# Performance work log

Hardware: AMD Instinct MI355X
Metric: run time of the kernel (lower is better)

The kernel has to match this reference:

```python
import jax, jax.numpy as jnp
import numpy as np

D_MODEL = 2048
N_HEADS = 16
D_HEAD = D_MODEL // N_HEADS
BATCH = 4
SEQ = 2048


def setup_inputs() -> dict:
    key = jax.random.key(0)
    ks = jax.random.split(key, 10)
    s = 1.0 / np.sqrt(D_MODEL)
    inp = {
        "x": jax.random.normal(ks[0], (BATCH, SEQ, D_MODEL), dtype=jnp.float32),
        "attn_mask": jnp.ones((1, 1, SEQ, SEQ), dtype=jnp.int32),
        "Wq": jax.random.uniform(ks[1], (D_MODEL, D_MODEL), jnp.float32, -s, s),
        "bq": jax.random.uniform(ks[2], (D_MODEL,), jnp.float32, -s, s),
        "Wk": jax.random.uniform(ks[3], (D_MODEL, D_MODEL), jnp.float32, -s, s),
        "bk": jax.random.uniform(ks[4], (D_MODEL,), jnp.float32, -s, s),
        "Wv": jax.random.uniform(ks[5], (D_MODEL, D_MODEL), jnp.float32, -s, s),
        "bv": jax.random.uniform(ks[6], (D_MODEL,), jnp.float32, -s, s),
        "Wo": jax.random.uniform(ks[7], (D_MODEL, D_MODEL), jnp.float32, -s, s),
        "bo": jax.random.uniform(ks[8], (D_MODEL,), jnp.float32, -s, s),
    }
    return inp


def reference(x, attn_mask, Wq, bq, Wk, bk, Wv, bv, Wo, bo):
    B, S, D = x.shape
    # projections (torch Linear: x @ W.T + b); split heads -> (B, H, S, Dh)
    def split(t):
        return t.reshape(B, S, N_HEADS, D_HEAD).transpose(0, 2, 1, 3)
    q = split(x @ Wq.T + bq)
    k = split(x @ Wk.T + bk)
    v = split(x @ Wv.T + bv)
    scale = 1.0 / np.sqrt(D_HEAD).astype(np.float32)
    scores = jnp.einsum('bhqd,bhkd->bhqk', q, k) * scale  # (B,H,S,S)
    scores = jnp.where(attn_mask == 0, jnp.float32(-jnp.inf), scores)
    attn = jax.nn.softmax(scores, axis=-1)
    out = jnp.einsum('bhqk,bhkd->bhqd', attn, v)  # (B,H,S,Dh)
    out = out.transpose(0, 2, 1, 3).reshape(B, S, D)
    return out @ Wo.T + bo
```

## Files before the change

### kernel.cpp

```cpp
#include <hip/hip_runtime.h>
#include <stdint.h>
#include <stddef.h>

typedef __attribute__((ext_vector_type(8))) short short8;
typedef __attribute__((ext_vector_type(4))) float f32x4;

#define SEQ    2048
#define DMODEL 2048
#define NHEAD  16
#define DHEAD  128
#define BATCH  4
#define KVT    32
#define NKVT   (SEQ / KVT)

__device__ __forceinline__ unsigned short f2b(float f) {
  unsigned int u;
  __builtin_memcpy(&u, &f, sizeof(u));
  u = u + 0x7FFFu + ((u >> 16) & 1u);
  return (unsigned short)(u >> 16);
}

__device__ __forceinline__ void gload16(const void* g, void* l) {
  __builtin_amdgcn_global_load_lds(
      (const __attribute__((address_space(1))) unsigned int*)g,
      (__attribute__((address_space(3))) unsigned int*)l, 16, 0, 0);
}

__global__ __launch_bounds__(256) void cvt_x_kernel(
    const float* __restrict__ src, unsigned short* __restrict__ dst, int n8)
{
  const int i = blockIdx.x * 256 + threadIdx.x;
  if (i >= n8) return;
  const f32x4 a = *(const f32x4*)(src + (size_t)i * 8);
  const f32x4 b = *(const f32x4*)(src + (size_t)i * 8 + 4);
  short8 o;
  o[0] = (short)f2b(a[0]); o[1] = (short)f2b(a[1]);
  o[2] = (short)f2b(a[2]); o[3] = (short)f2b(a[3]);
  o[4] = (short)f2b(b[0]); o[5] = (short)f2b(b[1]);
  o[6] = (short)f2b(b[2]); o[7] = (short)f2b(b[3]);
  *(short8*)(dst + (size_t)i * 8) = o;
}

__global__ __launch_bounds__(256) void cvt_w_kernel(
    const float* __restrict__ s0, const float* __restrict__ s1,
    const float* __restrict__ s2, const float* __restrict__ s3,
    unsigned short* __restrict__ dst, int n8)
{
  const int y = blockIdx.y;
  const float* src = (y == 0) ? s0 : (y == 1) ? s1 : (y == 2) ? s2 : s3;
  unsigned short* d = dst + (size_t)y * DMODEL * DMODEL;
  const int i = blockIdx.x * 256 + threadIdx.x;
  if (i >= n8) return;
  const f32x4 a = *(const f32x4*)(src + (size_t)i * 8);
  const f32x4 b = *(const f32x4*)(src + (size_t)i * 8 + 4);
  short8 o;
  o[0] = (short)f2b(a[0]); o[1] = (short)f2b(a[1]);
  o[2] = (short)f2b(a[2]); o[3] = (short)f2b(a[3]);
  o[4] = (short)f2b(b[0]); o[5] = (short)f2b(b[1]);
  o[6] = (short)f2b(b[2]); o[7] = (short)f2b(b[3]);
  *(short8*)(d + (size_t)i * 8) = o;
}

__global__ __launch_bounds__(256) void gemm_bt_kernel(
    const unsigned short* __restrict__ A,
    const unsigned short* __restrict__ W0, const unsigned short* __restrict__ W1,
    const unsigned short* __restrict__ W2,
    const float* __restrict__ b0, const float* __restrict__ b1,
    const float* __restrict__ b2,
    unsigned short* __restrict__ o0, unsigned short* __restrict__ o1,
    unsigned short* __restrict__ o2,
    float* __restrict__ of,
    int mode_base)
{
  const int z = blockIdx.z;
  const unsigned short* W    = (z == 0) ? W0 : (z == 1) ? W1 : W2;
  const float* bias          = (z == 0) ? b0 : (z == 1) ? b1 : b2;
  unsigned short* out        = (z == 0) ? o0 : (z == 1) ? o1 : o2;
  const int mode = mode_base + z;

  const int m0 = blockIdx.y * 128;
  const int n0 = blockIdx.x * 128;

  __shared__ __align__(16) unsigned short As[128 * 32];
  __shared__ __align__(16) unsigned short Bs[128 * 32];

  const int tid  = threadIdx.x;
  const int wave = tid >> 6;
  const int lane = tid & 63;
  const int l15  = lane & 15;
  const int lg   = lane >> 4;
  const int wr   = wave >> 1;
  const int wc   = wave & 1;

  f32x4 acc[4][4];
#pragma unroll
  for (int m = 0; m < 4; ++m)
#pragma unroll
    for (int n = 0; n < 4; ++n) acc[m][n] = (f32x4){0.f, 0.f, 0.f, 0.f};

  for (int kt = 0; kt < 64; ++kt) {
    const int k0 = kt * 32;
#pragma unroll
    for (int is = 0; is < 2; ++is) {
      const int f   = (is * 256 + tid) * 16;
      const int row = f >> 6;
      const int off = f & 63;
      gload16((const char*)(A + (size_t)(m0 + row) * DMODEL + k0) + off, (char*)As + f);
      gload16((const char*)(W + (size_t)(n0 + row) * DMODEL + k0) + off, (char*)Bs + f);
    }
    __syncthreads();

    short8 af[4], bfr[4];
#pragma unroll
    for (int m = 0; m < 4; ++m)
      af[m] = *(const short8*)(As + (wr * 64 + m * 16 + l15) * 32 + lg * 8);
#pragma unroll
    for (int n = 0; n < 4; ++n)
      bfr[n] = *(const short8*)(Bs + (wc * 64 + n * 16 + l15) * 32 + lg * 8);

#pragma unroll
    for (int m = 0; m < 4; ++m)
#pragma unroll
      for (int n = 0; n < 4; ++n)
        acc[m][n] = __builtin_amdgcn_mfma_f32_16x16x32_bf16(af[m], bfr[n], acc[m][n], 0, 0, 0);

    __syncthreads();
  }

#pragma unroll
  for (int n = 0; n < 4; ++n) {
    const int j = n0 + wc * 64 + n * 16 + l15;
    const float bb = bias[j];
#pragma unroll
    for (int m = 0; m < 4; ++m) {
#pragma unroll
      for (int r = 0; r < 4; ++r) {
        const int i = m0 + wr * 64 + m * 16 + lg * 4 + r;
        float v = acc[m][n][r] + bb;
        if (mode == 0) v *= 0.0883883476483184f;
        if (mode == 3) {
          of[(size_t)i * DMODEL + j] = v;
        } else {
          const int b = i >> 11, s = i & 2047, hh = j >> 7, dh = j & 127;
          const size_t bhOff = (size_t)(b * 16 + hh) * (SEQ * DHEAD);
          size_t addr;
          if (mode == 0)
            addr = bhOff + (size_t)s * DHEAD + dh;
          else if (mode == 1)
            addr = bhOff + (size_t)(s >> 4) * 2048 + (dh >> 5) * 512
                 + ((dh >> 3) & 3) * 128 + (s & 15) * 8 + (dh & 7);
          else
            addr = bhOff + (size_t)(s >> 5) * 4096 + (dh >> 4) * 512
                 + ((s >> 3) & 3) * 128 + (dh & 15) * 8 + (s & 7);
          out[addr] = f2b(v);
        }
      }
    }
  }
}

__global__ __launch_bounds__(256, 4) void attn_kernel(
    const unsigned short* __restrict__ Q,
    const unsigned short* __restrict__ Kf,
    const unsigned short* __restrict__ Vf,
    unsigned short* __restrict__ AO)
{
  const int idx = blockIdx.x;
  const int xcd = idx & 7;
  const int sq  = idx >> 3;
  const int bh  = xcd * 8 + (sq >> 5);
  const int qt  = sq & 31;

  const int wave = threadIdx.x >> 6;
  const int lane = threadIdx.x & 63;
  const int l15  = lane & 15;
  const int lg   = lane >> 4;
  const int q0   = qt * 64 + wave * 16;

  const unsigned short* Qb = Q  + (size_t)bh * SEQ * DHEAD;
  const unsigned short* Kb = Kf + (size_t)bh * SEQ * DHEAD;
  const unsigned short* Vb = Vf + (size_t)bh * SEQ * DHEAD;

  __shared__ __align__(16) unsigned short Ks[2][4096];
  __shared__ __align__(16) unsigned short Vs[2][4096];
  __shared__ __align__(16) unsigned short P[4][16][40];

  short8 qf[4];
#pragma unroll
  for (int k = 0; k < 4; ++k)
    qf[k] = *(const short8*)(Qb + (size_t)(q0 + l15) * DHEAD + k * 32 + lg * 8);

  short8 onesf;
#pragma unroll
  for (int e = 0; e < 8; ++e) onesf[e] = (short)0x3F80;

  f32x4 oacc[9];
#pragma unroll
  for (int n = 0; n < 9; ++n) oacc[n] = (f32x4){0.f, 0.f, 0.f, 0.f};
  float mrun[4];
#pragma unroll
  for (int r = 0; r < 4; ++r) mrun[r] = -1e30f;

  const int t = threadIdx.x;
  auto STAGE = [&](int buf, int kvt) {
    const unsigned short* ksrc = Kb + (size_t)kvt * 4096;
    const unsigned short* vsrc = Vb + (size_t)kvt * 4096;
    gload16(ksrc + t * 8,        &Ks[buf][t * 8]);
    gload16(ksrc + 2048 + t * 8, &Ks[buf][2048 + t * 8]);
    gload16(vsrc + t * 8,        &Vs[buf][t * 8]);
    gload16(vsrc + 2048 + t * 8, &Vs[buf][2048 + t * 8]);
  };

  STAGE(0, 0);

  for (int kvt = 0; kvt < NKVT; ++kvt) {
    const int cur = kvt & 1;
    if (kvt + 1 < NKVT) {
      STAGE(cur ^ 1, kvt + 1);
      asm volatile("s_waitcnt vmcnt(4)" ::: "memory");
    } else {
      asm volatile("s_waitcnt vmcnt(0)" ::: "memory");
    }
    __builtin_amdgcn_s_barrier();
    __builtin_amdgcn_sched_barrier(0);

    f32x4 sacc[2];
#pragma unroll
    for (int n = 0; n < 2; ++n) sacc[n] = (f32x4){0.f, 0.f, 0.f, 0.f};
    __builtin_amdgcn_s_setprio(1);
#pragma unroll
    for (int n = 0; n < 2; ++n) {
#pragma unroll
      for (int k = 0; k < 4; ++k) {
        short8 kfr = *(const short8*)(&Ks[cur][n * 2048 + k * 512 + lane * 8]);
        sacc[n] = __builtin_amdgcn_mfma_f32_16x16x32_bf16(qf[k], kfr, sacc[n], 0, 0, 0);
      }
    }
    __builtin_amdgcn_s_setprio(0);

    float d = -1e30f;
#pragma unroll
    for (int r = 0; r < 4; ++r)
      d = fmaxf(d, fmaxf(sacc[0][r], sacc[1][r]) - mrun[r]);
    if (__any(d > 8.f)) {
#pragma unroll
      for (int r = 0; r < 4; ++r) {
        float m = fmaxf(sacc[0][r], sacc[1][r]);
        m = fmaxf(m, __shfl_xor(m, 1));
        m = fmaxf(m, __shfl_xor(m, 2));
        m = fmaxf(m, __shfl_xor(m, 4));
        m = fmaxf(m, __shfl_xor(m, 8));
        if (m > mrun[r]) {
          const float alpha = __expf(mrun[r] - m);
#pragma unroll
          for (int n = 0; n < 9; ++n) oacc[n][r] *= alpha;
          mrun[r] = m;
        }
      }
    }

#pragma unroll
    for (int n = 0; n < 2; ++n)
#pragma unroll
      for (int r = 0; r < 4; ++r)
        P[wave][lg * 4 + r][n * 16 + l15] =
            (unsigned short)f2b(__expf(sacc[n][r] - mrun[r]));
    asm volatile("s_waitcnt lgkmcnt(0)" ::: "memory");
    __builtin_amdgcn_sched_barrier(0);

    short8 pf = *(const short8*)(&P[wave][l15][lg * 8]);
    __builtin_amdgcn_s_setprio(1);
#pragma unroll
    for (int n = 0; n < 8; ++n) {
      short8 vfr = *(const short8*)(&Vs[cur][n * 512 + lane * 8]);
      oacc[n] = __builtin_amdgcn_mfma_f32_16x16x32_bf16(pf, vfr, oacc[n], 0, 0, 0);
    }
    oacc[8] = __builtin_amdgcn_mfma_f32_16x16x32_bf16(pf, onesf, oacc[8], 0, 0, 0);
    __builtin_amdgcn_s_setprio(0);

    asm volatile("s_waitcnt lgkmcnt(0)" ::: "memory");
    __builtin_amdgcn_s_barrier();
    __builtin_amdgcn_sched_barrier(0);
  }

  const int b = bh >> 4, h = bh & 15;
  float inv[4];
#pragma unroll
  for (int r = 0; r < 4; ++r) inv[r] = 1.f / oacc[8][r];
#pragma unroll
  for (int n = 0; n < 8; ++n) {
#pragma unroll
    for (int r = 0; r < 4; ++r) {
      const int srow = q0 + lg * 4 + r;
      const size_t addr = ((size_t)(b * SEQ + srow)) * DMODEL + h * DHEAD + n * 16 + l15;
      AO[addr] = f2b(oacc[n][r] * inv[r]);
    }
  }
}

extern "C" void kernel_launch(void* const* d_in, const int* in_sizes, int n_in,
                              void* d_out, int out_size, void* d_ws, size_t ws_size,
                              hipStream_t stream)
{
  const float* xf  = (const float*)d_in[0];
  const float* Wqf = (const float*)d_in[2];
  const float* bq  = (const float*)d_in[3];
  const float* Wkf = (const float*)d_in[4];
  const float* bk  = (const float*)d_in[5];
  const float* Wvf = (const float*)d_in[6];
  const float* bv  = (const float*)d_in[7];
  const float* Wof = (const float*)d_in[8];
  const float* bo  = (const float*)d_in[9];
  float* out = (float*)d_out;

  const size_t QE = (size_t)64 * SEQ * DHEAD;
  const size_t WE = (size_t)DMODEL * DMODEL;

  unsigned short* Qw = (unsigned short*)d_out;
  unsigned short* Kw = Qw + QE;

  unsigned short* Vtw = (unsigned short*)d_ws;
  unsigned short* AOw = Vtw + QE;
  unsigned short* xb  = AOw + QE;
  unsigned short* Wb  = xb + QE;
  unsigned short* Wqb = Wb;
  unsigned short* Wkb = Wb + WE;
  unsigned short* Wvb = Wb + 2 * WE;
  unsigned short* Wob = Wb + 3 * WE;

  cvt_x_kernel<<<dim3((int)(QE / 8 / 256)), 256, 0, stream>>>(xf, xb, (int)(QE / 8));
  cvt_w_kernel<<<dim3((int)(WE / 8 / 256), 4), 256, 0, stream>>>(
      Wqf, Wkf, Wvf, Wof, Wb, (int)(WE / 8));

  gemm_bt_kernel<<<dim3(16, 64, 3), 256, 0, stream>>>(
      xb, Wqb, Wkb, Wvb, bq, bk, bv, Qw, Kw, Vtw, nullptr, 0);

  attn_kernel<<<dim3(2048), 256, 0, stream>>>(Qw, Kw, Vtw, AOw);

  gemm_bt_kernel<<<dim3(16, 64, 1), 256, 0, stream>>>(
      AOw, Wob, Wob, Wob, bo, bo, bo, nullptr, nullptr, nullptr, out, 3);
}
```

Baseline: 624.2 us.

## Use 256x256 pipelined GEMM tiles with fragment-major pretiled bf16 operand layout

```diff
diff --git a/kernel.cpp b/kernel.cpp
--- a/kernel.cpp
+++ b/kernel.cpp
@@ -26,19 +26,24 @@
       (__attribute__((address_space(3))) unsigned int*)l, 16, 0, 0);
 }
 
+
 __global__ __launch_bounds__(256) void cvt_x_kernel(
     const float* __restrict__ src, unsigned short* __restrict__ dst, int n8)
 {
-  const int i = blockIdx.x * 256 + threadIdx.x;
-  if (i >= n8) return;
-  const f32x4 a = *(const f32x4*)(src + (size_t)i * 8);
-  const f32x4 b = *(const f32x4*)(src + (size_t)i * 8 + 4);
+  const int idx = blockIdx.x * 256 + threadIdx.x;
+  if (idx >= n8) return;
+  const f32x4 a = *(const f32x4*)(src + (size_t)idx * 8);
+  const f32x4 b = *(const f32x4*)(src + (size_t)idx * 8 + 4);
   short8 o;
   o[0] = (short)f2b(a[0]); o[1] = (short)f2b(a[1]);
   o[2] = (short)f2b(a[2]); o[3] = (short)f2b(a[3]);
   o[4] = (short)f2b(b[0]); o[5] = (short)f2b(b[1]);
   o[6] = (short)f2b(b[2]); o[7] = (short)f2b(b[3]);
-  *(short8*)(dst + (size_t)i * 8) = o;
+  const int i = idx >> 8;
+  const int k = (idx & 255) * 8;
+  const size_t e = ((size_t)(i >> 4) * 64 + (k >> 5)) * 512
+                 + (((k >> 3) & 3) * 16 + (i & 15)) * 8;
+  *(short8*)(dst + e) = o;
 }
 
 __global__ __launch_bounds__(256) void cvt_w_kernel(
@@ -49,19 +54,23 @@
   const int y = blockIdx.y;
   const float* src = (y == 0) ? s0 : (y == 1) ? s1 : (y == 2) ? s2 : s3;
   unsigned short* d = dst + (size_t)y * DMODEL * DMODEL;
-  const int i = blockIdx.x * 256 + threadIdx.x;
-  if (i >= n8) return;
-  const f32x4 a = *(const f32x4*)(src + (size_t)i * 8);
-  const f32x4 b = *(const f32x4*)(src + (size_t)i * 8 + 4);
+  const int idx = blockIdx.x * 256 + threadIdx.x;
+  if (idx >= n8) return;
+  const f32x4 a = *(const f32x4*)(src + (size_t)idx * 8);
+  const f32x4 b = *(const f32x4*)(src + (size_t)idx * 8 + 4);
   short8 o;
   o[0] = (short)f2b(a[0]); o[1] = (short)f2b(a[1]);
   o[2] = (short)f2b(a[2]); o[3] = (short)f2b(a[3]);
   o[4] = (short)f2b(b[0]); o[5] = (short)f2b(b[1]);
   o[6] = (short)f2b(b[2]); o[7] = (short)f2b(b[3]);
-  *(short8*)(d + (size_t)i * 8) = o;
-}
-
-__global__ __launch_bounds__(256) void gemm_bt_kernel(
+  const int i = idx >> 8;
+  const int k = (idx & 255) * 8;
+  const size_t e = ((size_t)(i >> 4) * 64 + (k >> 5)) * 512
+                 + (((k >> 3) & 3) * 16 + (i & 15)) * 8;
+  *(short8*)(d + e) = o;
+}
+
+__global__ __launch_bounds__(512, 2) void gemm_bt_kernel(
     const unsigned short* __restrict__ A,
     const unsigned short* __restrict__ W0, const unsigned short* __restrict__ W1,
     const unsigned short* __restrict__ W2,
@@ -78,70 +87,105 @@
   unsigned short* out        = (z == 0) ? o0 : (z == 1) ? o1 : o2;
   const int mode = mode_base + z;
 
-  const int m0 = blockIdx.y * 128;
-  const int n0 = blockIdx.x * 128;
-
-  __shared__ __align__(16) unsigned short As[128 * 32];
-  __shared__ __align__(16) unsigned short Bs[128 * 32];
-
-  const int tid  = threadIdx.x;
-  const int wave = tid >> 6;
-  const int lane = tid & 63;
-  const int l15  = lane & 15;
-  const int lg   = lane >> 4;
-  const int wr   = wave >> 1;
-  const int wc   = wave & 1;
-
-  f32x4 acc[4][4];
-#pragma unroll
-  for (int m = 0; m < 4; ++m)
+  const int m0 = blockIdx.y * 256;
+  const int n0 = blockIdx.x * 256;
+
+  __shared__ __align__(16) unsigned short LA[4][8192];
+  __shared__ __align__(16) unsigned short LB[4][8192];
+
+  const int tid = threadIdx.x;
+  const int wid = tid >> 6;
+  const int ln  = tid & 63;
+  const int l15 = ln & 15;
+  const int lg  = ln >> 4;
+  const int wr  = wid >> 2;
+  const int wc  = wid & 3;
+
+  const int arow = m0 >> 4;
+  const int brow = n0 >> 4;
+
+  auto stageA = [&](int kt) {
+    const unsigned short* s = A + ((size_t)(arow + wid) * 64 + kt) * 512 + ln * 8;
+    unsigned short* d = &LA[kt & 3][wid * 512 + ln * 8];
+    gload16(s, d);
+    gload16(s + (size_t)8 * 64 * 512, d + 8 * 512);
+  };
+  auto stageB = [&](int kt) {
+    const unsigned short* s = W + ((size_t)(brow + wid) * 64 + kt) * 512 + ln * 8;
+    unsigned short* d = &LB[kt & 3][wid * 512 + ln * 8];
+    gload16(s, d);
+    gload16(s + (size_t)8 * 64 * 512, d + 8 * 512);
+  };
+
+  f32x4 acc[8][4];
+#pragma unroll
+  for (int m = 0; m < 8; ++m)
 #pragma unroll
     for (int n = 0; n < 4; ++n) acc[m][n] = (f32x4){0.f, 0.f, 0.f, 0.f};
 
-  for (int kt = 0; kt < 64; ++kt) {
-    const int k0 = kt * 32;
-#pragma unroll
-    for (int is = 0; is < 2; ++is) {
-      const int f   = (is * 256 + tid) * 16;
-      const int row = f >> 6;
-      const int off = f & 63;
-      gload16((const char*)(A + (size_t)(m0 + row) * DMODEL + k0) + off, (char*)As + f);
-      gload16((const char*)(W + (size_t)(n0 + row) * DMODEL + k0) + off, (char*)Bs + f);
-    }
-    __syncthreads();
-
-    short8 af[4], bfr[4];
-#pragma unroll
-    for (int m = 0; m < 4; ++m)
-      af[m] = *(const short8*)(As + (wr * 64 + m * 16 + l15) * 32 + lg * 8);
-#pragma unroll
-    for (int n = 0; n < 4; ++n)
-      bfr[n] = *(const short8*)(Bs + (wc * 64 + n * 16 + l15) * 32 + lg * 8);
-
-#pragma unroll
-    for (int m = 0; m < 4; ++m)
-#pragma unroll
-      for (int n = 0; n < 4; ++n)
-        acc[m][n] = __builtin_amdgcn_mfma_f32_16x16x32_bf16(af[m], bfr[n], acc[m][n], 0, 0, 0);
-
-    __syncthreads();
+  stageA(0); stageB(0); stageA(1); stageB(1); stageA(2); stageB(2);
+  asm volatile("s_waitcnt vmcnt(8)" ::: "memory");
+  __builtin_amdgcn_s_barrier();
+
+  for (int j = 0; j < 64; ++j) {
+    const int buf = j & 3;
+
+    short8 a[8], bA[2];
+#pragma unroll
+    for (int mi = 0; mi < 8; ++mi)
+      a[mi] = *(const short8*)(&LA[buf][(wr * 8 + mi) * 512 + ln * 8]);
+#pragma unroll
+    for (int ni = 0; ni < 2; ++ni)
+      bA[ni] = *(const short8*)(&LB[buf][(wc * 4 + ni) * 512 + ln * 8]);
+    if (j + 3 < 64) stageA(j + 3);
+    __builtin_amdgcn_s_barrier();
+    asm volatile("s_waitcnt lgkmcnt(0)" ::: "memory");
+    __builtin_amdgcn_sched_barrier(0);
+    __builtin_amdgcn_s_setprio(1);
+#pragma unroll
+    for (int mi = 0; mi < 8; ++mi)
+#pragma unroll
+      for (int ni = 0; ni < 2; ++ni)
+        acc[mi][ni] = __builtin_amdgcn_mfma_f32_16x16x32_bf16(a[mi], bA[ni], acc[mi][ni], 0, 0, 0);
+    __builtin_amdgcn_s_setprio(0);
+    __builtin_amdgcn_s_barrier();
+
+    short8 bB[2];
+#pragma unroll
+    for (int ni = 0; ni < 2; ++ni)
+      bB[ni] = *(const short8*)(&LB[buf][(wc * 4 + 2 + ni) * 512 + ln * 8]);
+    if (j + 3 < 64) stageB(j + 3);
+    __builtin_amdgcn_s_barrier();
+    asm volatile("s_waitcnt lgkmcnt(0)" ::: "memory");
+    __builtin_amdgcn_sched_barrier(0);
+    __builtin_amdgcn_s_setprio(1);
+#pragma unroll
+    for (int mi = 0; mi < 8; ++mi)
+#pragma unroll
+      for (int ni = 0; ni < 2; ++ni)
+        acc[mi][2 + ni] = __builtin_amdgcn_mfma_f32_16x16x32_bf16(a[mi], bB[ni], acc[mi][2 + ni], 0, 0, 0);
+    __builtin_amdgcn_s_setprio(0);
+    if (j <= 60)      asm volatile("s_waitcnt vmcnt(8)" ::: "memory");
+    else if (j == 61) asm volatile("s_waitcnt vmcnt(4)" ::: "memory");
+    else if (j == 62) asm volatile("s_waitcnt vmcnt(0)" ::: "memory");
+    __builtin_amdgcn_s_barrier();
   }
 
 #pragma unroll
   for (int n = 0; n < 4; ++n) {
-    const int j = n0 + wc * 64 + n * 16 + l15;
-    const float bb = bias[j];
-#pragma unroll
-    for (int m = 0; m < 4; ++m) {
+    const int jj = n0 + wc * 64 + n * 16 + l15;
+    const float bb = bias[jj];
+#pragma unroll
+    for (int m = 0; m < 8; ++m) {
 #pragma unroll
       for (int r = 0; r < 4; ++r) {
-        const int i = m0 + wr * 64 + m * 16 + lg * 4 + r;
+        const int i = m0 + wr * 128 + m * 16 + lg * 4 + r;
         float v = acc[m][n][r] + bb;
         if (mode == 0) v *= 0.0883883476483184f;
         if (mode == 3) {
-          of[(size_t)i * DMODEL + j] = v;
+          of[(size_t)i * DMODEL + jj] = v;
         } else {
-          const int b = i >> 11, s = i & 2047, hh = j >> 7, dh = j & 127;
+          const int b = i >> 11, s = i & 2047, hh = jj >> 7, dh = jj & 127;
           const size_t bhOff = (size_t)(b * 16 + hh) * (SEQ * DHEAD);
           size_t addr;
           if (mode == 0)
@@ -289,11 +333,14 @@
   for (int r = 0; r < 4; ++r) inv[r] = 1.f / oacc[8][r];
 #pragma unroll
   for (int n = 0; n < 8; ++n) {
+    const int kk  = h * 4 + (n >> 1);
+    const int sub = (n * 2 + (l15 >> 3)) & 3;
 #pragma unroll
     for (int r = 0; r < 4; ++r) {
-      const int srow = q0 + lg * 4 + r;
-      const size_t addr = ((size_t)(b * SEQ + srow)) * DMODEL + h * DHEAD + n * 16 + l15;
-      AO[addr] = f2b(oacc[n][r] * inv[r]);
+      const int i = b * SEQ + q0 + lg * 4 + r;
+      const size_t e = ((size_t)(i >> 4) * 64 + kk) * 512
+                     + sub * 128 + (i & 15) * 8 + (l15 & 7);
+      AO[e] = f2b(oacc[n][r] * inv[r]);
     }
   }
 }
@@ -332,11 +379,11 @@
   cvt_w_kernel<<<dim3((int)(WE / 8 / 256), 4), 256, 0, stream>>>(
       Wqf, Wkf, Wvf, Wof, Wb, (int)(WE / 8));
 
-  gemm_bt_kernel<<<dim3(16, 64, 3), 256, 0, stream>>>(
+  gemm_bt_kernel<<<dim3(8, 32, 3), 512, 0, stream>>>(
       xb, Wqb, Wkb, Wvb, bq, bk, bv, Qw, Kw, Vtw, nullptr, 0);
 
   attn_kernel<<<dim3(2048), 256, 0, stream>>>(Qw, Kw, Vtw, AOw);
 
-  gemm_bt_kernel<<<dim3(16, 64, 1), 256, 0, stream>>>(
+  gemm_bt_kernel<<<dim3(8, 32, 1), 512, 0, stream>>>(
       AOw, Wob, Wob, Wob, bo, bo, bo, nullptr, nullptr, nullptr, out, 3);
 }
```

Result: faster. 571.1 us (-8.5%).
